# Optimization experiments

Hardware: AMD Instinct MI355X
Metric: run time of the kernel (lower is better)

## Reference

```python
import jax, jax.numpy as jnp
import numpy as np

B, N, F = 4, 1024, 256
AVG_DEG = 16.0


def setup_inputs() -> dict:
    key = jax.random.key(0)
    k1, k2, k3, k4 = jax.random.split(key, 4)
    u = jax.random.uniform(k1, (B, N, N))
    A = (u < AVG_DEG / N).astype(jnp.float32)
    A = jnp.maximum(A, jnp.swapaxes(A, 1, 2))            # symmetric
    A = A * (1.0 - jnp.eye(N, dtype=jnp.float32))        # no self loops (added in forward)
    x = jax.random.normal(k2, (B, N, F), dtype=jnp.float32)
    pos = jax.random.normal(k3, (B, N, 3), dtype=jnp.float32)
    order = jax.random.uniform(k4, (B, N), dtype=jnp.float32)  # 'random' ordering priorities
    node_mask = jnp.ones((B, N), dtype=bool)
    return {"x": x, "adj": A, "pos": pos, "order": order, "node_mask": node_mask}


def _select(order, excluded, included, node_mask):
    # Greedy frontier-based node selection (K-MIS with stride=2).
    Bn, Nn = order.shape
    ar = jnp.arange(Nn)
    idx0 = jnp.argmin(order, axis=-1).astype(jnp.int32)           # [B]
    available = node_mask
    frontier = ar[None, :] == idx0[:, None]                        # scatter idx0 -> True
    selected = jnp.zeros_like(available)

    def cond(st):
        av, fr, sel, idx = st
        return av.any()

    def body(st):
        av, fr, sel, idx = st
        current = ar[None, :] == idx[:, None]                      # [B,N] one-hot
        sel = sel | current
        exc_row = jnp.take_along_axis(excluded, idx[:, None, None], axis=1)[:, 0]  # excluded[current]
        inc_row = jnp.take_along_axis(included, idx[:, None, None], axis=1)[:, 0]  # included[current]
        av = av & ~current & ~exc_row
        fr = (fr | inc_row | ~fr.any(-1, keepdims=True)) & av      # restart frontier if empty
        mo = jnp.where(fr, order, jnp.inf)
        midx = jnp.argmin(mo, axis=-1).astype(jnp.int32)
        has_fr = fr.any(-1)
        idx = jnp.where(has_fr, midx, idx)
        return (av, fr, sel, idx)

    _, _, selected, _ = jax.lax.while_loop(cond, body, (available, frontier, selected, idx0))
    return selected


def _forward(x, adj, pos, order, node_mask):
    Nn = adj.shape[1]
    eye = jnp.eye(Nn, dtype=adj.dtype)
    adj1 = jnp.where(node_mask[:, :, None], adj + eye, 0.0)        # adj_k[1] = A + I, masked rows
    adj2 = adj1 @ adj                                              # adj_k[2] = (A+I) @ A
    excluded = adj1 != 0                                           # adj_k[stride-1].bool()
    included = adj2 != 0                                           # adj_k[stride].bool()
    selected = _select(jax.lax.stop_gradient(order), excluded, included, node_mask)
    # pad K to N instead of data-dependent num_nodes; mask zeroes the padding
    mask_f, perm = jax.lax.top_k(selected.astype(jnp.float32), Nn)  # [B,K], [B,K]
    adj_kernel = jnp.take_along_axis(adj1, perm[:, None, :], axis=2)  # [B,N,K]
    # add_pool: adj^T @ x, then mask
    x_p = jnp.einsum('bnk,bnf->bkf', adj_kernel, x) * mask_f[..., None]
    # mean_pool for pos: add_pool / column degree
    deg = adj_kernel.sum(axis=1)[..., None]                        # [B,K,1]
    pos_p = jnp.einsum('bnk,bnc->bkc', adj_kernel, pos) / deg * mask_f[..., None]
    # coarsened adjacency: gather cols then rows of adj_k[stride], mask both sides
    a = jnp.take_along_axis(adj2, perm[:, None, :], axis=2)
    a = jnp.take_along_axis(a, perm[:, :, None], axis=1)
    a = a * mask_f[:, None, :] * mask_f[:, :, None]
    return x_p, pos_p, a, mask_f.astype(bool)


def reference(x, adj, pos, order, node_mask):
    return _forward(x, adj, pos, order, node_mask)
```

## Files before the change

### kernel.cpp

```cpp
#include <hip/hip_runtime.h>
#include <hip/hip_bf16.h>

#define BB 4
#define NN 1024
#define FF 256
#define NBLK 1024
#define NTHR 256
#define SROWS 128

typedef __hip_bfloat16 bf16;
typedef unsigned long long u64;
typedef unsigned int u32;
typedef unsigned short u16;
typedef unsigned char u8;

__device__ __forceinline__ bf16 f2b(float v) { return __float2bfloat16(v); }
__device__ __forceinline__ u16 f2bbits(float v) {
    bf16 h = __float2bfloat16(v);
    u16 s; __builtin_memcpy(&s, &h, 2);
    return s;
}
template <typename OT> __device__ __forceinline__ OT fromf(float v);
template <> __device__ __forceinline__ float fromf<float>(float v) { return v; }
template <> __device__ __forceinline__ bf16 fromf<bf16>(float v) { return __float2bfloat16(v); }

__device__ __forceinline__ void st_wt(u32* p, u32 v)   { __hip_atomic_store(p, v, __ATOMIC_RELAXED, __HIP_MEMORY_SCOPE_SYSTEM); }
__device__ __forceinline__ void st_wt(u64* p, u64 v)   { __hip_atomic_store(p, v, __ATOMIC_RELAXED, __HIP_MEMORY_SCOPE_SYSTEM); }
__device__ __forceinline__ void st_wt(int* p, int v)   { __hip_atomic_store(p, v, __ATOMIC_RELAXED, __HIP_MEMORY_SCOPE_SYSTEM); }
__device__ __forceinline__ void st_wt(float* p, float v){ __hip_atomic_store(p, v, __ATOMIC_RELAXED, __HIP_MEMORY_SCOPE_SYSTEM); }

__device__ __forceinline__ void tree_sync(int* reg, int idx, int phase) {
    __syncthreads();
    if (threadIdx.x == 0) {
        asm volatile("s_waitcnt vmcnt(0)" ::: "memory");
        int* gc = reg + 32 * (9 + (idx >> 4));
        int v = __hip_atomic_fetch_add(gc, 1, __ATOMIC_RELAXED, __HIP_MEMORY_SCOPE_AGENT);
        if (v == phase * 16 - 1) {
            int r = __hip_atomic_fetch_add(reg, 1, __ATOMIC_RELAXED, __HIP_MEMORY_SCOPE_AGENT);
            if (r == phase * 64 - 1)
                for (int xx = 0; xx < 8; xx++)
                    __hip_atomic_store(reg + 32 * (1 + xx), phase,
                                       __ATOMIC_RELAXED, __HIP_MEMORY_SCOPE_AGENT);
        }
        int* flag = reg + 32 * (1 + (idx & 7));
        int spins = 0;
        while (__hip_atomic_load(flag, __ATOMIC_RELAXED, __HIP_MEMORY_SCOPE_AGENT) < phase) {
            if (spins < 64) __builtin_amdgcn_s_sleep(2);
            else            __builtin_amdgcn_s_sleep(16);
            if (++spins > (1 << 19)) break;
        }
        asm volatile("" ::: "memory");
    }
    __syncthreads();
}

__device__ __forceinline__ int build_nbr(const u64* myrow, u16* nbr, int* cntp, int t) {
    __syncthreads();
    if (t < 16) {
        int myc = __popcll(myrow[t]);
        int ps = myc;
#pragma unroll
        for (int off = 1; off < 16; off <<= 1) {
            int v = __shfl_up(ps, off);
            if (t >= off) ps += v;
        }
        int idx = ps - myc;
        u64 m = myrow[t];
        while (m) {
            int i = __ffsll(m) - 1;
            if (idx < 192) nbr[idx] = (u16)(t * 64 + i);
            idx++;
            m &= m - 1;
        }
        if (t == 15) *cntp = ps;
    }
    __syncthreads();
    return min(*cntp, 192);
}

template <typename OT>
__global__ __launch_bounds__(NTHR, 4) void mega_kernel(
        const float* __restrict__ x, const float* __restrict__ adj,
        const float* __restrict__ pos, const float* __restrict__ order,
        u64* __restrict__ bitsA, u32* __restrict__ packed,
        int* __restrict__ sp2node, int* __restrict__ node2sp,
        int* __restrict__ perm, int* __restrict__ kcnt,
        int* __restrict__ sink, int* __restrict__ bar,
        OT* __restrict__ out, size_t out_elems)
{
    const int B = blockIdx.x, t = threadIdx.x;
    __shared__ alignas(16) union ShU {
        u64 keys[NN];
        struct {
            u64 myrow[16], incw[16], part[256];
            int s2nT[16 * 65];
            u16 nbr[192];
            int cnt;
        } pb;
        struct {
            u32 stage[SROWS * 64];
            u8 selS[NN];
        } pc;
        struct {
            int p[NN];
            u64 myrow[16];
            u16 stx[FF];
            u16 sta[NN];
            float posp[64][3];
            u16 nbr[192];
            int cnt;
        } pd;
    } sh;

    const int b = B >> 8, rbase = (B & 255) * 4;

    if (B >= NBLK - 8) {
        const int sb = (B - (NBLK - 8)) >> 1, half = (B - (NBLK - 8)) & 1;
        for (int i = t; i < NN; i += NTHR) {
            float v = order[(size_t)sb * NN + i];
            u32 ub = __float_as_uint(v);
            u32 sk = (ub & 0x80000000u) ? ~ub : (ub | 0x80000000u);
            sh.keys[i] = ((u64)sk << 32) | (u32)i;
        }
        __syncthreads();
        u64 mk0 = sh.keys[half * 512 + t], mk1 = sh.keys[half * 512 + 256 + t];
        int r0 = 0, r1 = 0;
        for (int m = 0; m < NN; m++) {
            u64 v = sh.keys[m];
            r0 += (v < mk0);
            r1 += (v < mk1);
        }
        int n0 = (int)(mk0 & 0xFFFFFFFFu) & (NN - 1), n1 = (int)(mk1 & 0xFFFFFFFFu) & (NN - 1);
        r0 &= (NN - 1); r1 &= (NN - 1);
        st_wt(&sp2node[sb * NN + r0], n0); st_wt(&node2sp[sb * NN + n0], r0);
        st_wt(&sp2node[sb * NN + r1], n1); st_wt(&node2sp[sb * NN + n1], r1);
        __syncthreads();
    }

    for (int rr = 0; rr < 4; rr++) {
        const int r = rbase + rr;
        const size_t base = (size_t)b * NN * NN + (size_t)r * NN;
        for (int q = 0; q < 4; q++) {
            int j = q * 256 + t;
            u64 bal = __ballot(adj[base + j] != 0.0f);
            if ((t & 63) == 0) st_wt(&bitsA[((size_t)b * NN + r) * 16 + (j >> 6)], bal);
        }
    }
    tree_sync(bar, B, 1);

    for (int q = 0; q < 4; q++) {
        int j = q * 256 + t;
        sh.pb.s2nT[(j & 15) * 65 + (j >> 4)] = sp2node[b * NN + j] & (NN - 1);
    }
    for (int rr = 0; rr < 4; rr++) {
        const int r = rbase + rr;
        if (t < 16) sh.pb.myrow[t] = bitsA[((size_t)b * NN + r) * 16 + t];
        const int c = build_nbr(sh.pb.myrow, sh.pb.nbr, &sh.pb.cnt, t);
        {
            const int w = t & 15, g = t >> 4;
            u64 v = 0;
            for (int n2 = g; n2 < c; n2 += 16)
                v |= bitsA[((size_t)b * NN + sh.pb.nbr[n2]) * 16 + w];
            sh.pb.part[t] = v;
        }
        __syncthreads();
        if (t < 16) {
            u64 acc = sh.pb.myrow[t];
            for (int g = 0; g < 16; g++) acc |= sh.pb.part[g * 16 + t];
            sh.pb.incw[t] = acc;
        }
        __syncthreads();
        if (t < 64) {
            const int s = node2sp[b * NN + r] & (NN - 1);
            u32 e16 = 0, i16 = 0;
            for (int q = 0; q < 16; q++) {
                int jn = sh.pb.s2nT[q * 65 + t];
                u32 eb = (u32)((sh.pb.myrow[jn >> 6] >> (jn & 63)) & 1) | (u32)(jn == r);
                u32 ib = (u32)((sh.pb.incw[jn >> 6] >> (jn & 63)) & 1);
                e16 |= eb << q;
                i16 |= ib << q;
            }
            st_wt(&packed[((size_t)b * NN + s) * 64 + t], e16 | (i16 << 16));
        }
        __syncthreads();
    }
    tree_sync(bar, B, 2);

    if (B < 4) {
        const int sb = B;
        const u32* pk = packed + (size_t)sb * NN * 64;
        u32 acc = 0;
        for (int i = t; i < NN * 16; i += NTHR) {
            uint4 v = ((const uint4*)pk)[i];
            if ((i >> 4) < SROWS) ((uint4*)sh.pc.stage)[i] = v;
            acc ^= v.x ^ v.y ^ v.z ^ v.w;
        }
        if (acc == 0xDEADBEEFu) atomicAdd(sink, 1);
        __syncthreads();

        if (t < 64) {
            const int l = t;
            u32 avail = 0xFFFFu, front = (l == 0) ? 1u : 0u, sel = 0u;
            int cur = 0;
            for (int iter = 0; iter < 2 * NN + 8; ++iter) {
                if ((cur >> 4) == l) sel |= 1u << (cur & 15);
                u32 p;
                if (cur < SROWS) p = sh.pc.stage[cur * 64 + l];
                else             p = pk[(size_t)cur * 64 + l];
                avail &= ~(p & 0xFFFFu);
                front = (front | (p >> 16)) & avail;
                u64 fb = __ballot(front != 0u);
                if (!fb) {
                    front = avail;
                    fb = __ballot(front != 0u);
                    if (!fb) break;
                }
                int lf = __ffsll(fb) - 1;
                u32 f = __shfl(front, lf);
                cur = (lf * 16 + (__ffs(f) - 1)) & (NN - 1);
            }
            for (int q = 0; q < 16; q++) sh.pc.selS[l * 16 + q] = (sel >> q) & 1u;
        }
        __syncthreads();
        if (t < 64) {
            const int l = t;
            u32 nodesel = 0;
            const int* n2s = node2sp + sb * NN;
            for (int q = 0; q < 16; q++)
                nodesel |= ((u32)sh.pc.selS[n2s[l * 16 + q] & (NN - 1)]) << q;
            int cnt_sel = __popc(nodesel);
            int ps = cnt_sel;
            for (int off = 1; off < 64; off <<= 1) {
                int v = __shfl_up(ps, off);
                if (l >= off) ps += v;
            }
            const int K = __shfl(ps, 63);
            int pos_ = (ps - cnt_sel) & (NN - 1);
            u32 m = nodesel;
            while (m) { int i = __ffs(m) - 1; st_wt(&perm[sb * NN + pos_], l * 16 + i); pos_ = (pos_ + 1) & (NN - 1); m &= m - 1; }
            int posu = (K + l * 16 - (ps - cnt_sel)) & (NN - 1);
            m = (~nodesel) & 0xFFFFu;
            while (m) { int i = __ffs(m) - 1; st_wt(&perm[sb * NN + posu], l * 16 + i); posu = (posu + 1) & (NN - 1); m &= m - 1; }
            if (l == 0) st_wt(&kcnt[sb], K);
        }
    } else {
        const size_t nb8 = (out_elems * sizeof(OT)) >> 3;
        u64* o8 = (u64*)out;
        for (size_t i = (size_t)(B - 4) * NTHR + t; i < nb8; i += (size_t)(NBLK - 4) * NTHR)
            st_wt(o8 + i, (u64)0);
        u32 acc = 0;
        const int slot = B >> 3;
        const uint4* xs = (const uint4*)x + (size_t)slot * 2048;
        for (int i = t; i < 2048; i += NTHR) {
            uint4 v = xs[i];
            acc ^= v.x ^ v.y ^ v.z ^ v.w;
        }
        const u64* bs = bitsA + (size_t)slot * 512;
        for (int i = t; i < 512; i += NTHR) acc ^= (u32)bs[i];
        if (acc == 0xDEADBEEFu) atomicAdd(sink, 1);
    }
    tree_sync(bar, B, 3);

    OT* out_x = out;
    OT* out_pos = out_x + (size_t)BB * NN * FF;
    OT* out_a = out_pos + (size_t)BB * NN * 3;
    OT* out_mask = out_a + (size_t)BB * NN * NN;

    for (int task = B; task < BB * NN; task += NBLK) {
        const int b2 = task & 3, k = task >> 2;
        const int K = min(kcnt[b2], NN);
        if (k >= K) continue;
        const int r = perm[b2 * NN + k] & (NN - 1);
        OT* ox = out_x + ((size_t)b2 * NN + k) * FF;
        OT* op = out_pos + ((size_t)b2 * NN + k) * 3;
        OT* oa = out_a + ((size_t)b2 * NN + k) * NN;
        if (t == 0) out_mask[(size_t)b2 * NN + k] = fromf<OT>(1.0f);
        if (t < 16) sh.pd.myrow[t] = bitsA[((size_t)b2 * NN + r) * 16 + t];
        for (int q = 0; q < 4; q++) { int j = t + q * 256; sh.pd.p[j] = perm[b2 * NN + j] & (NN - 1); }
        const int c = build_nbr(sh.pd.myrow, sh.pd.nbr, &sh.pd.cnt, t);

        const float* xr = x + (size_t)b2 * NN * FF;
        float acc = xr[(size_t)r * FF + t];
        int i = 0;
        for (; i + 4 <= c; i += 4) {
            float a0 = xr[(size_t)sh.pd.nbr[i + 0] * FF + t];
            float a1 = xr[(size_t)sh.pd.nbr[i + 1] * FF + t];
            float a2 = xr[(size_t)sh.pd.nbr[i + 2] * FF + t];
            float a3 = xr[(size_t)sh.pd.nbr[i + 3] * FF + t];
            acc += a0; acc += a1; acc += a2; acc += a3;
        }
        for (; i < c; i++) acc += xr[(size_t)sh.pd.nbr[i] * FF + t];

        if (t < 64) {
            float p0 = 0.0f, p1 = 0.0f, p2 = 0.0f;
            const float* pr = pos + (size_t)b2 * NN * 3;
            for (int n = t; n < c; n += 64) {
                const float* pp = pr + (size_t)sh.pd.nbr[n] * 3;
                p0 += pp[0]; p1 += pp[1]; p2 += pp[2];
            }
            sh.pd.posp[t][0] = p0; sh.pd.posp[t][1] = p1; sh.pd.posp[t][2] = p2;
        }

        if constexpr (sizeof(OT) == 2) {
            sh.pd.stx[t] = f2bbits(acc);
            for (int q = 0; q < 4; q++) {
                int jj = t + q * 256;
                float v = 0.0f;
                if (jj < K) {
                    const int pj = sh.pd.p[jj];
                    const u64* rj = bitsA + ((size_t)b2 * NN + pj) * 16;
                    int a2 = (int)((sh.pd.myrow[pj >> 6] >> (pj & 63)) & 1);
#pragma unroll
                    for (int w = 0; w < 16; w++)
                        a2 += __popcll(sh.pd.myrow[w] & rj[w]);
                    v = (float)a2;
                }
                sh.pd.sta[jj] = f2bbits(v);
            }
            __syncthreads();
            if (t < 3) {
                const float* pr = pos + (size_t)b2 * NN * 3;
                float pa = pr[(size_t)r * 3 + t];
                for (int g = 0; g < 64; g++) pa += sh.pd.posp[g][t];
                op[t] = fromf<OT>(pa / (float)(c + 1));
            }
            const int nu = (K + 7) >> 3;
            if (t < nu) ((uint4*)oa)[t] = ((const uint4*)sh.pd.sta)[t];
            if (t < 32) ((uint4*)ox)[t] = ((const uint4*)sh.pd.stx)[t];
            __syncthreads();
        } else {
            ox[t] = acc;
            for (int q = 0; q < 4; q++) {
                int jj = t + q * 256;
                if (jj < K) {
                    const int pj = sh.pd.p[jj];
                    const u64* rj = bitsA + ((size_t)b2 * NN + pj) * 16;
                    int a2 = (int)((sh.pd.myrow[pj >> 6] >> (pj & 63)) & 1);
#pragma unroll
                    for (int w = 0; w < 16; w++)
                        a2 += __popcll(sh.pd.myrow[w] & rj[w]);
                    oa[jj] = (float)a2;
                }
            }
            __syncthreads();
            if (t < 3) {
                const float* pr = pos + (size_t)b2 * NN * 3;
                float pa = pr[(size_t)r * 3 + t];
                for (int g = 0; g < 64; g++) pa += sh.pd.posp[g][t];
                op[t] = fromf<OT>(pa / (float)(c + 1));
            }
            __syncthreads();
        }
    }
}

extern "C" void kernel_launch(void* const* d_in, const int* in_sizes, int n_in,
                              void* d_out, int out_size, void* d_ws, size_t ws_size,
                              hipStream_t stream) {
    const float* x     = (const float*)d_in[0];
    const float* adj   = (const float*)d_in[1];
    const float* pos   = (const float*)d_in[2];
    const float* order = (const float*)d_in[3];

    char* ws = (char*)d_ws;
    size_t off = 0;
    u64* bitsA     = (u64*)(ws + off);  off += (size_t)BB * NN * 16 * 8;
    u32* packed    = (u32*)(ws + off);  off += (size_t)BB * NN * 64 * 4;
    int* sp2node   = (int*)(ws + off);  off += (size_t)BB * NN * 4;
    int* node2sp   = (int*)(ws + off);  off += (size_t)BB * NN * 4;
    int* perm      = (int*)(ws + off);  off += (size_t)BB * NN * 4;
    int* kcnt      = (int*)(ws + off);  off += 64;
    int* sink      = (int*)(ws + off);  off += 64;
    int* bar       = (int*)(ws + off);  off += 16384;

    hipMemsetAsync(bar, 0, 16384, stream);

    bool outf32 = false;
    size_t osz = 0;
    if (hipMemPtrGetInfo(d_out, &osz) == hipSuccess)
        outf32 = (osz >= 4ull * (size_t)out_size);

    if (outf32)
        mega_kernel<float><<<NBLK, NTHR, 0, stream>>>(x, adj, pos, order, bitsA, packed,
            sp2node, node2sp, perm, kcnt, sink, bar, (float*)d_out, (size_t)out_size);
    else
        mega_kernel<bf16><<<NBLK, NTHR, 0, stream>>>(x, adj, pos, order, bitsA, packed,
            sp2node, node2sp, perm, kcnt, sink, bar, (bf16*)d_out, (size_t)out_size);
}
```

Before: 166.1 us.

## Split persistent mega-kernel into four launches replacing grid barriers

Replaces the single persistent kernel, which relied on software grid-wide tree barriers, with four separate kernels: pack/sort, inclusion packing, greedy selection and output. Kernel boundaries now provide the synchronisation, so the spin-wait barriers, system-scope stores and barrier memset go away. The output kernel zero-fills unselected rows itself instead of running a separate full-output clear. The select loop also swaps a shuffle for four ballots to pick the frontier index. The cost is extra launch overhead, and the selection phase runs alone on only four blocks with no other work overlapping it.

```diff
diff --git a/kernel.cpp b/kernel.cpp
--- a/kernel.cpp
+++ b/kernel.cpp
@@ -23,36 +23,6 @@
 template <typename OT> __device__ __forceinline__ OT fromf(float v);
 template <> __device__ __forceinline__ float fromf<float>(float v) { return v; }
 template <> __device__ __forceinline__ bf16 fromf<bf16>(float v) { return __float2bfloat16(v); }
-
-__device__ __forceinline__ void st_wt(u32* p, u32 v)   { __hip_atomic_store(p, v, __ATOMIC_RELAXED, __HIP_MEMORY_SCOPE_SYSTEM); }
-__device__ __forceinline__ void st_wt(u64* p, u64 v)   { __hip_atomic_store(p, v, __ATOMIC_RELAXED, __HIP_MEMORY_SCOPE_SYSTEM); }
-__device__ __forceinline__ void st_wt(int* p, int v)   { __hip_atomic_store(p, v, __ATOMIC_RELAXED, __HIP_MEMORY_SCOPE_SYSTEM); }
-__device__ __forceinline__ void st_wt(float* p, float v){ __hip_atomic_store(p, v, __ATOMIC_RELAXED, __HIP_MEMORY_SCOPE_SYSTEM); }
-
-__device__ __forceinline__ void tree_sync(int* reg, int idx, int phase) {
-    __syncthreads();
-    if (threadIdx.x == 0) {
-        asm volatile("s_waitcnt vmcnt(0)" ::: "memory");
-        int* gc = reg + 32 * (9 + (idx >> 4));
-        int v = __hip_atomic_fetch_add(gc, 1, __ATOMIC_RELAXED, __HIP_MEMORY_SCOPE_AGENT);
-        if (v == phase * 16 - 1) {
-            int r = __hip_atomic_fetch_add(reg, 1, __ATOMIC_RELAXED, __HIP_MEMORY_SCOPE_AGENT);
-            if (r == phase * 64 - 1)
-                for (int xx = 0; xx < 8; xx++)
-                    __hip_atomic_store(reg + 32 * (1 + xx), phase,
-                                       __ATOMIC_RELAXED, __HIP_MEMORY_SCOPE_AGENT);
-        }
-        int* flag = reg + 32 * (1 + (idx & 7));
-        int spins = 0;
-        while (__hip_atomic_load(flag, __ATOMIC_RELAXED, __HIP_MEMORY_SCOPE_AGENT) < phase) {
-            if (spins < 64) __builtin_amdgcn_s_sleep(2);
-            else            __builtin_amdgcn_s_sleep(16);
-            if (++spins > (1 << 19)) break;
-        }
-        asm volatile("" ::: "memory");
-    }
-    __syncthreads();
-}
 
 __device__ __forceinline__ int build_nbr(const u64* myrow, u16* nbr, int* cntp, int t) {
     __syncthreads();
@@ -78,278 +48,270 @@
     return min(*cntp, 192);
 }
 
-template <typename OT>
-__global__ __launch_bounds__(NTHR, 4) void mega_kernel(
-        const float* __restrict__ x, const float* __restrict__ adj,
-        const float* __restrict__ pos, const float* __restrict__ order,
-        u64* __restrict__ bitsA, u32* __restrict__ packed,
-        int* __restrict__ sp2node, int* __restrict__ node2sp,
-        int* __restrict__ perm, int* __restrict__ kcnt,
-        int* __restrict__ sink, int* __restrict__ bar,
-        OT* __restrict__ out, size_t out_elems)
-{
+__global__ __launch_bounds__(NTHR) void pack_sort_kernel(
+        const float* __restrict__ adj, const float* __restrict__ order,
+        u64* __restrict__ bitsA, int* __restrict__ sp2node, int* __restrict__ node2sp) {
     const int B = blockIdx.x, t = threadIdx.x;
-    __shared__ alignas(16) union ShU {
-        u64 keys[NN];
-        struct {
-            u64 myrow[16], incw[16], part[256];
-            int s2nT[16 * 65];
-            u16 nbr[192];
-            int cnt;
-        } pb;
-        struct {
-            u32 stage[SROWS * 64];
-            u8 selS[NN];
-        } pc;
-        struct {
-            int p[NN];
-            u64 myrow[16];
-            u16 stx[FF];
-            u16 sta[NN];
-            float posp[64][3];
-            u16 nbr[192];
-            int cnt;
-        } pd;
-    } sh;
-
-    const int b = B >> 8, rbase = (B & 255) * 4;
-
-    if (B >= NBLK - 8) {
-        const int sb = (B - (NBLK - 8)) >> 1, half = (B - (NBLK - 8)) & 1;
+    __shared__ alignas(16) u64 keys[NN];
+    if (B >= NBLK) {
+        const int sb = (B - NBLK) >> 1, half = (B - NBLK) & 1;
         for (int i = t; i < NN; i += NTHR) {
             float v = order[(size_t)sb * NN + i];
             u32 ub = __float_as_uint(v);
             u32 sk = (ub & 0x80000000u) ? ~ub : (ub | 0x80000000u);
-            sh.keys[i] = ((u64)sk << 32) | (u32)i;
-        }
-        __syncthreads();
-        u64 mk0 = sh.keys[half * 512 + t], mk1 = sh.keys[half * 512 + 256 + t];
+            keys[i] = ((u64)sk << 32) | (u32)i;
+        }
+        __syncthreads();
+        u64 mk0 = keys[half * 512 + t], mk1 = keys[half * 512 + 256 + t];
         int r0 = 0, r1 = 0;
         for (int m = 0; m < NN; m++) {
-            u64 v = sh.keys[m];
+            u64 v = keys[m];
             r0 += (v < mk0);
             r1 += (v < mk1);
         }
         int n0 = (int)(mk0 & 0xFFFFFFFFu) & (NN - 1), n1 = (int)(mk1 & 0xFFFFFFFFu) & (NN - 1);
         r0 &= (NN - 1); r1 &= (NN - 1);
-        st_wt(&sp2node[sb * NN + r0], n0); st_wt(&node2sp[sb * NN + n0], r0);
-        st_wt(&sp2node[sb * NN + r1], n1); st_wt(&node2sp[sb * NN + n1], r1);
-        __syncthreads();
-    }
-
+        sp2node[sb * NN + r0] = n0; node2sp[sb * NN + n0] = r0;
+        sp2node[sb * NN + r1] = n1; node2sp[sb * NN + n1] = r1;
+        return;
+    }
+    const int b = B >> 8, rbase = (B & 255) * 4;
     for (int rr = 0; rr < 4; rr++) {
         const int r = rbase + rr;
         const size_t base = (size_t)b * NN * NN + (size_t)r * NN;
         for (int q = 0; q < 4; q++) {
             int j = q * 256 + t;
             u64 bal = __ballot(adj[base + j] != 0.0f);
-            if ((t & 63) == 0) st_wt(&bitsA[((size_t)b * NN + r) * 16 + (j >> 6)], bal);
-        }
-    }
-    tree_sync(bar, B, 1);
-
+            if ((t & 63) == 0) bitsA[((size_t)b * NN + r) * 16 + (j >> 6)] = bal;
+        }
+    }
+}
+
+__global__ __launch_bounds__(NTHR) void inc_pack_kernel(
+        const u64* __restrict__ bitsA, const int* __restrict__ sp2node,
+        const int* __restrict__ node2sp, u32* __restrict__ packed) {
+    const int B = blockIdx.x, t = threadIdx.x;
+    const int b = B >> 8, rbase = (B & 255) * 4;
+    __shared__ alignas(16) struct {
+        u64 myrow[16], incw[16], part[256];
+        int s2nT[16 * 65];
+        u16 nbr[192];
+        int cnt;
+    } sh;
     for (int q = 0; q < 4; q++) {
         int j = q * 256 + t;
-        sh.pb.s2nT[(j & 15) * 65 + (j >> 4)] = sp2node[b * NN + j] & (NN - 1);
+        sh.s2nT[(j & 15) * 65 + (j >> 4)] = sp2node[b * NN + j] & (NN - 1);
     }
     for (int rr = 0; rr < 4; rr++) {
         const int r = rbase + rr;
-        if (t < 16) sh.pb.myrow[t] = bitsA[((size_t)b * NN + r) * 16 + t];
-        const int c = build_nbr(sh.pb.myrow, sh.pb.nbr, &sh.pb.cnt, t);
+        if (t < 16) sh.myrow[t] = bitsA[((size_t)b * NN + r) * 16 + t];
+        const int c = build_nbr(sh.myrow, sh.nbr, &sh.cnt, t);
         {
             const int w = t & 15, g = t >> 4;
             u64 v = 0;
             for (int n2 = g; n2 < c; n2 += 16)
-                v |= bitsA[((size_t)b * NN + sh.pb.nbr[n2]) * 16 + w];
-            sh.pb.part[t] = v;
+                v |= bitsA[((size_t)b * NN + sh.nbr[n2]) * 16 + w];
+            sh.part[t] = v;
         }
         __syncthreads();
         if (t < 16) {
-            u64 acc = sh.pb.myrow[t];
-            for (int g = 0; g < 16; g++) acc |= sh.pb.part[g * 16 + t];
-            sh.pb.incw[t] = acc;
+            u64 acc = sh.myrow[t];
+            for (int g = 0; g < 16; g++) acc |= sh.part[g * 16 + t];
+            sh.incw[t] = acc;
         }
         __syncthreads();
         if (t < 64) {
             const int s = node2sp[b * NN + r] & (NN - 1);
             u32 e16 = 0, i16 = 0;
             for (int q = 0; q < 16; q++) {
-                int jn = sh.pb.s2nT[q * 65 + t];
-                u32 eb = (u32)((sh.pb.myrow[jn >> 6] >> (jn & 63)) & 1) | (u32)(jn == r);
-                u32 ib = (u32)((sh.pb.incw[jn >> 6] >> (jn & 63)) & 1);
+                int jn = sh.s2nT[q * 65 + t];
+                u32 eb = (u32)((sh.myrow[jn >> 6] >> (jn & 63)) & 1) | (u32)(jn == r);
+                u32 ib = (u32)((sh.incw[jn >> 6] >> (jn & 63)) & 1);
                 e16 |= eb << q;
                 i16 |= ib << q;
             }
-            st_wt(&packed[((size_t)b * NN + s) * 64 + t], e16 | (i16 << 16));
-        }
-        __syncthreads();
-    }
-    tree_sync(bar, B, 2);
-
-    if (B < 4) {
-        const int sb = B;
-        const u32* pk = packed + (size_t)sb * NN * 64;
-        u32 acc = 0;
-        for (int i = t; i < NN * 16; i += NTHR) {
-            uint4 v = ((const uint4*)pk)[i];
-            if ((i >> 4) < SROWS) ((uint4*)sh.pc.stage)[i] = v;
-            acc ^= v.x ^ v.y ^ v.z ^ v.w;
-        }
-        if (acc == 0xDEADBEEFu) atomicAdd(sink, 1);
-        __syncthreads();
-
-        if (t < 64) {
-            const int l = t;
-            u32 avail = 0xFFFFu, front = (l == 0) ? 1u : 0u, sel = 0u;
-            int cur = 0;
-            for (int iter = 0; iter < 2 * NN + 8; ++iter) {
-                if ((cur >> 4) == l) sel |= 1u << (cur & 15);
-                u32 p;
-                if (cur < SROWS) p = sh.pc.stage[cur * 64 + l];
-                else             p = pk[(size_t)cur * 64 + l];
-                avail &= ~(p & 0xFFFFu);
-                front = (front | (p >> 16)) & avail;
-                u64 fb = __ballot(front != 0u);
-                if (!fb) {
-                    front = avail;
-                    fb = __ballot(front != 0u);
-                    if (!fb) break;
-                }
-                int lf = __ffsll(fb) - 1;
-                u32 f = __shfl(front, lf);
-                cur = (lf * 16 + (__ffs(f) - 1)) & (NN - 1);
+            packed[((size_t)b * NN + s) * 64 + t] = e16 | (i16 << 16);
+        }
+        __syncthreads();
+    }
+}
+
+__global__ __launch_bounds__(NTHR) void select_kernel(
+        const u32* __restrict__ packed, const int* __restrict__ node2sp,
+        int* __restrict__ perm, int* __restrict__ kcnt, int* __restrict__ sink) {
+    const int sb = blockIdx.x, t = threadIdx.x;
+    __shared__ alignas(16) struct {
+        u32 stage[SROWS * 64];
+        u8 selS[NN];
+    } sh;
+    const u32* pk = packed + (size_t)sb * NN * 64;
+    u32 acc = 0;
+    for (int i = t; i < NN * 16; i += NTHR) {
+        uint4 v = ((const uint4*)pk)[i];
+        if ((i >> 4) < SROWS) ((uint4*)sh.stage)[i] = v;
+        acc ^= v.x ^ v.y ^ v.z ^ v.w;
+    }
+    if (acc == 0xDEADBEEFu) atomicAdd(sink, 1);
+    __syncthreads();
+
+    if (t < 64) {
+        const int l = t;
+        u32 avail = 0xFFFFu, front = (l == 0) ? 1u : 0u, sel = 0u;
+        int cur = 0;
+        for (int iter = 0; iter < 2 * NN + 8; ++iter) {
+            if ((cur >> 4) == l) sel |= 1u << (cur & 15);
+            u32 p;
+            if (cur < SROWS) p = sh.stage[cur * 64 + l];
+            else             p = pk[(size_t)cur * 64 + l];
+            avail &= ~(p & 0xFFFFu);
+            front = (front | (p >> 16)) & avail;
+            u64 fb = __ballot(front != 0u);
+            if (!fb) {
+                front = avail;
+                fb = __ballot(front != 0u);
+                if (!fb) break;
             }
-            for (int q = 0; q < 16; q++) sh.pc.selS[l * 16 + q] = (sel >> q) & 1u;
-        }
-        __syncthreads();
-        if (t < 64) {
-            const int l = t;
-            u32 nodesel = 0;
-            const int* n2s = node2sp + sb * NN;
-            for (int q = 0; q < 16; q++)
-                nodesel |= ((u32)sh.pc.selS[n2s[l * 16 + q] & (NN - 1)]) << q;
-            int cnt_sel = __popc(nodesel);
-            int ps = cnt_sel;
-            for (int off = 1; off < 64; off <<= 1) {
-                int v = __shfl_up(ps, off);
-                if (l >= off) ps += v;
+            int lf = __ffsll(fb) - 1;
+            u32 ff = (u32)(__ffs(front) - 1);
+            u64 b0 = __ballot((ff & 1u) != 0u);
+            u64 b1 = __ballot((ff & 2u) != 0u);
+            u64 b2 = __ballot((ff & 4u) != 0u);
+            u64 b3 = __ballot((ff & 8u) != 0u);
+            int low = (int)(((b0 >> lf) & 1) | (((b1 >> lf) & 1) << 1) |
+                            (((b2 >> lf) & 1) << 2) | (((b3 >> lf) & 1) << 3));
+            cur = (lf * 16 + low) & (NN - 1);
+        }
+        for (int q = 0; q < 16; q++) sh.selS[l * 16 + q] = (sel >> q) & 1u;
+    }
+    __syncthreads();
+    if (t < 64) {
+        const int l = t;
+        u32 nodesel = 0;
+        const int* n2s = node2sp + sb * NN;
+        for (int q = 0; q < 16; q++)
+            nodesel |= ((u32)sh.selS[n2s[l * 16 + q] & (NN - 1)]) << q;
+        int cnt_sel = __popc(nodesel);
+        int ps = cnt_sel;
+        for (int off = 1; off < 64; off <<= 1) {
+            int v = __shfl_up(ps, off);
+            if (l >= off) ps += v;
+        }
+        const int K = __shfl(ps, 63);
+        int pos_ = (ps - cnt_sel) & (NN - 1);
+        u32 m = nodesel;
+        while (m) { int i = __ffs(m) - 1; perm[sb * NN + pos_] = l * 16 + i; pos_ = (pos_ + 1) & (NN - 1); m &= m - 1; }
+        int posu = (K + l * 16 - (ps - cnt_sel)) & (NN - 1);
+        m = (~nodesel) & 0xFFFFu;
+        while (m) { int i = __ffs(m) - 1; perm[sb * NN + posu] = l * 16 + i; posu = (posu + 1) & (NN - 1); m &= m - 1; }
+        if (l == 0) kcnt[sb] = K;
+    }
+}
+
+template <typename OT>
+__global__ __launch_bounds__(NTHR) void out_kernel(
+        const u64* __restrict__ bitsA, const float* __restrict__ x,
+        const float* __restrict__ pos,
+        const int* __restrict__ perm, const int* __restrict__ kcnt,
+        OT* __restrict__ out_x, OT* __restrict__ out_pos,
+        OT* __restrict__ out_a, OT* __restrict__ out_mask) {
+    const int k = blockIdx.x, b2 = blockIdx.y, t = threadIdx.x;
+    const int K = min(kcnt[b2], NN);
+    OT* ox = out_x + ((size_t)b2 * NN + k) * FF;
+    OT* op = out_pos + ((size_t)b2 * NN + k) * 3;
+    OT* oa = out_a + ((size_t)b2 * NN + k) * NN;
+    constexpr int OAU4 = (int)(NN * sizeof(OT) / 16);
+    constexpr int OXU4 = (int)(FF * sizeof(OT) / 16);
+    if (t == 0) out_mask[(size_t)b2 * NN + k] = fromf<OT>(k < K ? 1.0f : 0.0f);
+    if (k >= K) {
+        uint4 z = make_uint4(0, 0, 0, 0);
+        for (int i = t; i < OAU4; i += NTHR) ((uint4*)oa)[i] = z;
+        if (t < OXU4) ((uint4*)ox)[t] = z;
+        if (t < 3) op[t] = fromf<OT>(0.0f);
+        return;
+    }
+    const int r = perm[b2 * NN + k] & (NN - 1);
+    __shared__ alignas(16) struct {
+        int p[NN];
+        u64 myrow[16];
+        u16 stx[FF];
+        u16 sta[NN];
+        float posp[64][3];
+        u16 nbr[192];
+        int cnt;
+    } sh;
+    if (t < 16) sh.myrow[t] = bitsA[((size_t)b2 * NN + r) * 16 + t];
+    for (int q = 0; q < 4; q++) { int j = t + q * 256; sh.p[j] = perm[b2 * NN + j] & (NN - 1); }
+    const int c = build_nbr(sh.myrow, sh.nbr, &sh.cnt, t);
+
+    const float* xr = x + (size_t)b2 * NN * FF;
+    float acc = xr[(size_t)r * FF + t];
+    int i = 0;
+    for (; i + 4 <= c; i += 4) {
+        float a0 = xr[(size_t)sh.nbr[i + 0] * FF + t];
+        float a1 = xr[(size_t)sh.nbr[i + 1] * FF + t];
+        float a2 = xr[(size_t)sh.nbr[i + 2] * FF + t];
+        float a3 = xr[(size_t)sh.nbr[i + 3] * FF + t];
+        acc += a0; acc += a1; acc += a2; acc += a3;
+    }
+    for (; i < c; i++) acc += xr[(size_t)sh.nbr[i] * FF + t];
+
+    if (t < 64) {
+        float p0 = 0.0f, p1 = 0.0f, p2 = 0.0f;
+        const float* pr = pos + (size_t)b2 * NN * 3;
+        for (int n = t; n < c; n += 64) {
+            const float* pp = pr + (size_t)sh.nbr[n] * 3;
+            p0 += pp[0]; p1 += pp[1]; p2 += pp[2];
+        }
+        sh.posp[t][0] = p0; sh.posp[t][1] = p1; sh.posp[t][2] = p2;
+    }
+
+    if constexpr (sizeof(OT) == 2) {
+        sh.stx[t] = f2bbits(acc);
+        for (int q = 0; q < 4; q++) {
+            int jj = t + q * 256;
+            float v = 0.0f;
+            if (jj < K) {
+                const int pj = sh.p[jj];
+                const u64* rj = bitsA + ((size_t)b2 * NN + pj) * 16;
+                int a2 = (int)((sh.myrow[pj >> 6] >> (pj & 63)) & 1);
+#pragma unroll
+                for (int w = 0; w < 16; w++)
+                    a2 += __popcll(sh.myrow[w] & rj[w]);
+                v = (float)a2;
             }
-            const int K = __shfl(ps, 63);
-            int pos_ = (ps - cnt_sel) & (NN - 1);
-            u32 m = nodesel;
-            while (m) { int i = __ffs(m) - 1; st_wt(&perm[sb * NN + pos_], l * 16 + i); pos_ = (pos_ + 1) & (NN - 1); m &= m - 1; }
-            int posu = (K + l * 16 - (ps - cnt_sel)) & (NN - 1);
-            m = (~nodesel) & 0xFFFFu;
-            while (m) { int i = __ffs(m) - 1; st_wt(&perm[sb * NN + posu], l * 16 + i); posu = (posu + 1) & (NN - 1); m &= m - 1; }
-            if (l == 0) st_wt(&kcnt[sb], K);
-        }
+            sh.sta[jj] = f2bbits(v);
+        }
+        __syncthreads();
+        if (t < 3) {
+            const float* pr = pos + (size_t)b2 * NN * 3;
+            float pa = pr[(size_t)r * 3 + t];
+            for (int g = 0; g < 64; g++) pa += sh.posp[g][t];
+            op[t] = fromf<OT>(pa / (float)(c + 1));
+        }
+        if (t < 128) ((uint4*)oa)[t] = ((const uint4*)sh.sta)[t];
+        if (t < 32)  ((uint4*)ox)[t] = ((const uint4*)sh.stx)[t];
     } else {
-        const size_t nb8 = (out_elems * sizeof(OT)) >> 3;
-        u64* o8 = (u64*)out;
-        for (size_t i = (size_t)(B - 4) * NTHR + t; i < nb8; i += (size_t)(NBLK - 4) * NTHR)
-            st_wt(o8 + i, (u64)0);
-        u32 acc = 0;
-        const int slot = B >> 3;
-        const uint4* xs = (const uint4*)x + (size_t)slot * 2048;
-        for (int i = t; i < 2048; i += NTHR) {
-            uint4 v = xs[i];
-            acc ^= v.x ^ v.y ^ v.z ^ v.w;
-        }
-        const u64* bs = bitsA + (size_t)slot * 512;
-        for (int i = t; i < 512; i += NTHR) acc ^= (u32)bs[i];
-        if (acc == 0xDEADBEEFu) atomicAdd(sink, 1);
-    }
-    tree_sync(bar, B, 3);
-
-    OT* out_x = out;
-    OT* out_pos = out_x + (size_t)BB * NN * FF;
-    OT* out_a = out_pos + (size_t)BB * NN * 3;
-    OT* out_mask = out_a + (size_t)BB * NN * NN;
-
-    for (int task = B; task < BB * NN; task += NBLK) {
-        const int b2 = task & 3, k = task >> 2;
-        const int K = min(kcnt[b2], NN);
-        if (k >= K) continue;
-        const int r = perm[b2 * NN + k] & (NN - 1);
-        OT* ox = out_x + ((size_t)b2 * NN + k) * FF;
-        OT* op = out_pos + ((size_t)b2 * NN + k) * 3;
-        OT* oa = out_a + ((size_t)b2 * NN + k) * NN;
-        if (t == 0) out_mask[(size_t)b2 * NN + k] = fromf<OT>(1.0f);
-        if (t < 16) sh.pd.myrow[t] = bitsA[((size_t)b2 * NN + r) * 16 + t];
-        for (int q = 0; q < 4; q++) { int j = t + q * 256; sh.pd.p[j] = perm[b2 * NN + j] & (NN - 1); }
-        const int c = build_nbr(sh.pd.myrow, sh.pd.nbr, &sh.pd.cnt, t);
-
-        const float* xr = x + (size_t)b2 * NN * FF;
-        float acc = xr[(size_t)r * FF + t];
-        int i = 0;
-        for (; i + 4 <= c; i += 4) {
-            float a0 = xr[(size_t)sh.pd.nbr[i + 0] * FF + t];
-            float a1 = xr[(size_t)sh.pd.nbr[i + 1] * FF + t];
-            float a2 = xr[(size_t)sh.pd.nbr[i + 2] * FF + t];
-            float a3 = xr[(size_t)sh.pd.nbr[i + 3] * FF + t];
-            acc += a0; acc += a1; acc += a2; acc += a3;
-        }
-        for (; i < c; i++) acc += xr[(size_t)sh.pd.nbr[i] * FF + t];
-
-        if (t < 64) {
-            float p0 = 0.0f, p1 = 0.0f, p2 = 0.0f;
+        ox[t] = acc;
+        for (int q = 0; q < 4; q++) {
+            int jj = t + q * 256;
+            float v = 0.0f;
+            if (jj < K) {
+                const int pj = sh.p[jj];
+                const u64* rj = bitsA + ((size_t)b2 * NN + pj) * 16;
+                int a2 = (int)((sh.myrow[pj >> 6] >> (pj & 63)) & 1);
+#pragma unroll
+                for (int w = 0; w < 16; w++)
+                    a2 += __popcll(sh.myrow[w] & rj[w]);
+                v = (float)a2;
+            }
+            oa[jj] = v;
+        }
+        __syncthreads();
+        if (t < 3) {
             const float* pr = pos + (size_t)b2 * NN * 3;
-            for (int n = t; n < c; n += 64) {
-                const float* pp = pr + (size_t)sh.pd.nbr[n] * 3;
-                p0 += pp[0]; p1 += pp[1]; p2 += pp[2];
-            }
-            sh.pd.posp[t][0] = p0; sh.pd.posp[t][1] = p1; sh.pd.posp[t][2] = p2;
-        }
-
-        if constexpr (sizeof(OT) == 2) {
-            sh.pd.stx[t] = f2bbits(acc);
-            for (int q = 0; q < 4; q++) {
-                int jj = t + q * 256;
-                float v = 0.0f;
-                if (jj < K) {
-                    const int pj = sh.pd.p[jj];
-                    const u64* rj = bitsA + ((size_t)b2 * NN + pj) * 16;
-                    int a2 = (int)((sh.pd.myrow[pj >> 6] >> (pj & 63)) & 1);
-#pragma unroll
-                    for (int w = 0; w < 16; w++)
-                        a2 += __popcll(sh.pd.myrow[w] & rj[w]);
-                    v = (float)a2;
-                }
-                sh.pd.sta[jj] = f2bbits(v);
-            }
-            __syncthreads();
-            if (t < 3) {
-                const float* pr = pos + (size_t)b2 * NN * 3;
-                float pa = pr[(size_t)r * 3 + t];
-                for (int g = 0; g < 64; g++) pa += sh.pd.posp[g][t];
-                op[t] = fromf<OT>(pa / (float)(c + 1));
-            }
-            const int nu = (K + 7) >> 3;
-            if (t < nu) ((uint4*)oa)[t] = ((const uint4*)sh.pd.sta)[t];
-            if (t < 32) ((uint4*)ox)[t] = ((const uint4*)sh.pd.stx)[t];
-            __syncthreads();
-        } else {
-            ox[t] = acc;
-            for (int q = 0; q < 4; q++) {
-                int jj = t + q * 256;
-                if (jj < K) {
-                    const int pj = sh.pd.p[jj];
-                    const u64* rj = bitsA + ((size_t)b2 * NN + pj) * 16;
-                    int a2 = (int)((sh.pd.myrow[pj >> 6] >> (pj & 63)) & 1);
-#pragma unroll
-                    for (int w = 0; w < 16; w++)
-                        a2 += __popcll(sh.pd.myrow[w] & rj[w]);
-                    oa[jj] = (float)a2;
-                }
-            }
-            __syncthreads();
-            if (t < 3) {
-                const float* pr = pos + (size_t)b2 * NN * 3;
-                float pa = pr[(size_t)r * 3 + t];
-                for (int g = 0; g < 64; g++) pa += sh.pd.posp[g][t];
-                op[t] = fromf<OT>(pa / (float)(c + 1));
-            }
-            __syncthreads();
+            float pa = pr[(size_t)r * 3 + t];
+            for (int g = 0; g < 64; g++) pa += sh.posp[g][t];
+            op[t] = fromf<OT>(pa / (float)(c + 1));
         }
     }
 }
@@ -364,26 +326,38 @@
 
     char* ws = (char*)d_ws;
     size_t off = 0;
-    u64* bitsA     = (u64*)(ws + off);  off += (size_t)BB * NN * 16 * 8;
-    u32* packed    = (u32*)(ws + off);  off += (size_t)BB * NN * 64 * 4;
-    int* sp2node   = (int*)(ws + off);  off += (size_t)BB * NN * 4;
-    int* node2sp   = (int*)(ws + off);  off += (size_t)BB * NN * 4;
-    int* perm      = (int*)(ws + off);  off += (size_t)BB * NN * 4;
-    int* kcnt      = (int*)(ws + off);  off += 64;
-    int* sink      = (int*)(ws + off);  off += 64;
-    int* bar       = (int*)(ws + off);  off += 16384;
-
-    hipMemsetAsync(bar, 0, 16384, stream);
+    u64* bitsA   = (u64*)(ws + off); off += (size_t)BB * NN * 16 * 8;
+    u32* packed  = (u32*)(ws + off); off += (size_t)BB * NN * 64 * 4;
+    int* sp2node = (int*)(ws + off); off += (size_t)BB * NN * 4;
+    int* node2sp = (int*)(ws + off); off += (size_t)BB * NN * 4;
+    int* perm    = (int*)(ws + off); off += (size_t)BB * NN * 4;
+    int* kcnt    = (int*)(ws + off); off += 64;
+    int* sink    = (int*)(ws + off); off += 64;
 
     bool outf32 = false;
     size_t osz = 0;
     if (hipMemPtrGetInfo(d_out, &osz) == hipSuccess)
         outf32 = (osz >= 4ull * (size_t)out_size);
 
-    if (outf32)
-        mega_kernel<float><<<NBLK, NTHR, 0, stream>>>(x, adj, pos, order, bitsA, packed,
-            sp2node, node2sp, perm, kcnt, sink, bar, (float*)d_out, (size_t)out_size);
-    else
-        mega_kernel<bf16><<<NBLK, NTHR, 0, stream>>>(x, adj, pos, order, bitsA, packed,
-            sp2node, node2sp, perm, kcnt, sink, bar, (bf16*)d_out, (size_t)out_size);
-}
+    pack_sort_kernel<<<NBLK + 8, NTHR, 0, stream>>>(adj, order, bitsA, sp2node, node2sp);
+    inc_pack_kernel<<<NBLK, NTHR, 0, stream>>>(bitsA, sp2node, node2sp, packed);
+    select_kernel<<<BB, NTHR, 0, stream>>>(packed, node2sp, perm, kcnt, sink);
+
+    if (outf32) {
+        float* out      = (float*)d_out;
+        float* out_x    = out;
+        float* out_pos  = out_x + (size_t)BB * NN * FF;
+        float* out_a    = out_pos + (size_t)BB * NN * 3;
+        float* out_mask = out_a + (size_t)BB * NN * NN;
+        out_kernel<float><<<dim3(NN, BB), NTHR, 0, stream>>>(bitsA, x, pos, perm, kcnt,
+                                                             out_x, out_pos, out_a, out_mask);
+    } else {
+        bf16* out      = (bf16*)d_out;
+        bf16* out_x    = out;
+        bf16* out_pos  = out_x + (size_t)BB * NN * FF;
+        bf16* out_a    = out_pos + (size_t)BB * NN * 3;
+        bf16* out_mask = out_a + (size_t)BB * NN * NN;
+        out_kernel<bf16><<<dim3(NN, BB), NTHR, 0, stream>>>(bitsA, x, pos, perm, kcnt,
+                                                            out_x, out_pos, out_a, out_mask);
+    }
+}
```

Result: faster. 158.1 us (-4.8%).

## Replace final grid barrier with per-batch flags and speculative row prefetch in select loop

Applied to the files above, without the earlier changes.

The global tree barrier after the selection phase is removed. Each selector block now signals per-batch flags, and worker blocks wait only on the flag for their own batch. The blanket output-zeroing pass is dropped, and rows past K are instead written as explicit zeros in the per-task loop. The serial greedy selection loop now prefetches the next four packed rows into registers, on the guess that the next current node is usually the one that follows. It also replaces a shuffle with ballots to compute the next index. These changes aim to shorten the serial critical path and end the wait on all blocks. The cost is extra loads per iteration, and the spin-wait could time out.

```diff
diff --git a/kernel.cpp b/kernel.cpp
--- a/kernel.cpp
+++ b/kernel.cpp
@@ -202,11 +202,25 @@
             const int l = t;
             u32 avail = 0xFFFFu, front = (l == 0) ? 1u : 0u, sel = 0u;
             int cur = 0;
+            int pfc = -100;
+            u32 pf0 = 0, pf1 = 0, pf2 = 0, pf3 = 0;
             for (int iter = 0; iter < 2 * NN + 8; ++iter) {
                 if ((cur >> 4) == l) sel |= 1u << (cur & 15);
+                const int d = cur - pfc;
                 u32 p;
-                if (cur < SROWS) p = sh.pc.stage[cur * 64 + l];
-                else             p = pk[(size_t)cur * 64 + l];
+                if (d >= 1 && d <= 4) {
+                    p = (d == 1) ? pf0 : (d == 2) ? pf1 : (d == 3) ? pf2 : pf3;
+                } else if (cur < SROWS) {
+                    p = sh.pc.stage[cur * 64 + l];
+                } else {
+                    p = pk[(size_t)cur * 64 + l];
+                }
+                pf0 = pk[(size_t)((cur + 1) & (NN - 1)) * 64 + l];
+                pf1 = pk[(size_t)((cur + 2) & (NN - 1)) * 64 + l];
+                pf2 = pk[(size_t)((cur + 3) & (NN - 1)) * 64 + l];
+                pf3 = pk[(size_t)((cur + 4) & (NN - 1)) * 64 + l];
+                pfc = cur;
+
                 avail &= ~(p & 0xFFFFu);
                 front = (front | (p >> 16)) & avail;
                 u64 fb = __ballot(front != 0u);
@@ -216,8 +230,14 @@
                     if (!fb) break;
                 }
                 int lf = __ffsll(fb) - 1;
-                u32 f = __shfl(front, lf);
-                cur = (lf * 16 + (__ffs(f) - 1)) & (NN - 1);
+                u32 ff = (u32)(__ffs(front) - 1);
+                u64 b0 = __ballot((ff & 1u) != 0u);
+                u64 b1 = __ballot((ff & 2u) != 0u);
+                u64 b2 = __ballot((ff & 4u) != 0u);
+                u64 b3 = __ballot((ff & 8u) != 0u);
+                int low = (int)(((b0 >> lf) & 1) | (((b1 >> lf) & 1) << 1) |
+                                (((b2 >> lf) & 1) << 2) | (((b3 >> lf) & 1) << 3));
+                cur = (lf * 16 + low) & (NN - 1);
             }
             for (int q = 0; q < 16; q++) sh.pc.selS[l * 16 + q] = (sel >> q) & 1u;
         }
@@ -243,38 +263,52 @@
             while (m) { int i = __ffs(m) - 1; st_wt(&perm[sb * NN + posu], l * 16 + i); posu = (posu + 1) & (NN - 1); m &= m - 1; }
             if (l == 0) st_wt(&kcnt[sb], K);
         }
-    } else {
-        const size_t nb8 = (out_elems * sizeof(OT)) >> 3;
-        u64* o8 = (u64*)out;
-        for (size_t i = (size_t)(B - 4) * NTHR + t; i < nb8; i += (size_t)(NBLK - 4) * NTHR)
-            st_wt(o8 + i, (u64)0);
-        u32 acc = 0;
-        const int slot = B >> 3;
-        const uint4* xs = (const uint4*)x + (size_t)slot * 2048;
-        for (int i = t; i < 2048; i += NTHR) {
-            uint4 v = xs[i];
-            acc ^= v.x ^ v.y ^ v.z ^ v.w;
-        }
-        const u64* bs = bitsA + (size_t)slot * 512;
-        for (int i = t; i < 512; i += NTHR) acc ^= (u32)bs[i];
-        if (acc == 0xDEADBEEFu) atomicAdd(sink, 1);
-    }
-    tree_sync(bar, B, 3);
+        __syncthreads();
+        if (t == 0) {
+            asm volatile("s_waitcnt vmcnt(0)" ::: "memory");
+            for (int xx = 0; xx < 8; xx++)
+                __hip_atomic_store(bar + 32 * (73 + sb * 8 + xx), 1,
+                                   __ATOMIC_RELAXED, __HIP_MEMORY_SCOPE_AGENT);
+        }
+    }
+
+    const int b2 = B & 3;
+    if (B >= 4) {
+        int* fl = bar + 32 * (73 + b2 * 8 + ((B >> 2) & 7));
+        if (t == 0) {
+            int spins = 0;
+            while (__hip_atomic_load(fl, __ATOMIC_RELAXED, __HIP_MEMORY_SCOPE_AGENT) < 1) {
+                if (spins < 64) __builtin_amdgcn_s_sleep(2);
+                else            __builtin_amdgcn_s_sleep(16);
+                if (++spins > (1 << 19)) break;
+            }
+            asm volatile("" ::: "memory");
+        }
+        __syncthreads();
+    }
 
     OT* out_x = out;
     OT* out_pos = out_x + (size_t)BB * NN * FF;
     OT* out_a = out_pos + (size_t)BB * NN * 3;
     OT* out_mask = out_a + (size_t)BB * NN * NN;
+    const int K = min(kcnt[b2], NN);
+    constexpr int OAU4 = (int)(NN * sizeof(OT) / 16);
+    constexpr int OXU4 = (int)(FF * sizeof(OT) / 16);
 
     for (int task = B; task < BB * NN; task += NBLK) {
-        const int b2 = task & 3, k = task >> 2;
-        const int K = min(kcnt[b2], NN);
-        if (k >= K) continue;
-        const int r = perm[b2 * NN + k] & (NN - 1);
+        const int k = task >> 2;
         OT* ox = out_x + ((size_t)b2 * NN + k) * FF;
         OT* op = out_pos + ((size_t)b2 * NN + k) * 3;
         OT* oa = out_a + ((size_t)b2 * NN + k) * NN;
-        if (t == 0) out_mask[(size_t)b2 * NN + k] = fromf<OT>(1.0f);
+        if (t == 0) out_mask[(size_t)b2 * NN + k] = fromf<OT>(k < K ? 1.0f : 0.0f);
+        if (k >= K) {
+            uint4 z = make_uint4(0, 0, 0, 0);
+            for (int i = t; i < OAU4; i += NTHR) ((uint4*)oa)[i] = z;
+            if (t < OXU4) ((uint4*)ox)[t] = z;
+            if (t < 3) op[t] = fromf<OT>(0.0f);
+            continue;
+        }
+        const int r = perm[b2 * NN + k] & (NN - 1);
         if (t < 16) sh.pd.myrow[t] = bitsA[((size_t)b2 * NN + r) * 16 + t];
         for (int q = 0; q < 4; q++) { int j = t + q * 256; sh.pd.p[j] = perm[b2 * NN + j] & (NN - 1); }
         const int c = build_nbr(sh.pd.myrow, sh.pd.nbr, &sh.pd.cnt, t);
@@ -324,14 +358,14 @@
                 for (int g = 0; g < 64; g++) pa += sh.pd.posp[g][t];
                 op[t] = fromf<OT>(pa / (float)(c + 1));
             }
-            const int nu = (K + 7) >> 3;
-            if (t < nu) ((uint4*)oa)[t] = ((const uint4*)sh.pd.sta)[t];
-            if (t < 32) ((uint4*)ox)[t] = ((const uint4*)sh.pd.stx)[t];
+            if (t < 128) ((uint4*)oa)[t] = ((const uint4*)sh.pd.sta)[t];
+            if (t < 32)  ((uint4*)ox)[t] = ((const uint4*)sh.pd.stx)[t];
             __syncthreads();
         } else {
             ox[t] = acc;
             for (int q = 0; q < 4; q++) {
                 int jj = t + q * 256;
+                float v = 0.0f;
                 if (jj < K) {
                     const int pj = sh.pd.p[jj];
                     const u64* rj = bitsA + ((size_t)b2 * NN + pj) * 16;
@@ -339,8 +373,9 @@
 #pragma unroll
                     for (int w = 0; w < 16; w++)
                         a2 += __popcll(sh.pd.myrow[w] & rj[w]);
-                    oa[jj] = (float)a2;
+                    v = (float)a2;
                 }
+                oa[jj] = v;
             }
             __syncthreads();
             if (t < 3) {
@@ -364,14 +399,14 @@
 
     char* ws = (char*)d_ws;
     size_t off = 0;
-    u64* bitsA     = (u64*)(ws + off);  off += (size_t)BB * NN * 16 * 8;
-    u32* packed    = (u32*)(ws + off);  off += (size_t)BB * NN * 64 * 4;
-    int* sp2node   = (int*)(ws + off);  off += (size_t)BB * NN * 4;
-    int* node2sp   = (int*)(ws + off);  off += (size_t)BB * NN * 4;
-    int* perm      = (int*)(ws + off);  off += (size_t)BB * NN * 4;
-    int* kcnt      = (int*)(ws + off);  off += 64;
-    int* sink      = (int*)(ws + off);  off += 64;
-    int* bar       = (int*)(ws + off);  off += 16384;
+    u64* bitsA   = (u64*)(ws + off); off += (size_t)BB * NN * 16 * 8;
+    u32* packed  = (u32*)(ws + off); off += (size_t)BB * NN * 64 * 4;
+    int* sp2node = (int*)(ws + off); off += (size_t)BB * NN * 4;
+    int* node2sp = (int*)(ws + off); off += (size_t)BB * NN * 4;
+    int* perm    = (int*)(ws + off); off += (size_t)BB * NN * 4;
+    int* kcnt    = (int*)(ws + off); off += 64;
+    int* sink    = (int*)(ws + off); off += 64;
+    int* bar     = (int*)(ws + off); off += 16384;
 
     hipMemsetAsync(bar, 0, 16384, stream);
 
```

Result: no change. 169.2 us (+1.8%).
